# Performance work log

Measured on AMD Instinct MI355X. Metric: run time of the kernel, lower is better.

## Reference

```python
import jax, jax.numpy as jnp
import numpy as np

B, N, F_IN, F_OUT = 8, 256, 64, 64
EPS = 1e-12


def _mlp(x, w1, b1, w2, b2):
    # Dense -> ReLU -> Dense -> ReLU
    h = jax.nn.relu(x @ w1 + b1)
    return jax.nn.relu(h @ w2 + b2)


def setup_inputs() -> dict:
    key = jax.random.key(0)
    ks = jax.random.split(key, 11)
    A = jax.random.uniform(ks[0], (B, N, N), dtype=jnp.float32)
    W = jax.random.normal(ks[1], (B, N, N, F_OUT), dtype=jnp.float32)
    x = jax.random.normal(ks[2], (B, N, F_IN), dtype=jnp.float32)
    sc_in = 1.0 / np.sqrt(F_IN)
    sc_out = 1.0 / np.sqrt(F_OUT)
    return {
        "A": A, "W": W, "x": x,
        # n_func params
        "n_w1": jax.random.normal(ks[3], (F_IN, F_OUT), dtype=jnp.float32) * sc_in,
        "n_b1": jnp.zeros((F_OUT,), dtype=jnp.float32),
        "n_w2": jax.random.normal(ks[4], (F_OUT, F_OUT), dtype=jnp.float32) * sc_out,
        "n_b2": jnp.zeros((F_OUT,), dtype=jnp.float32),
        # n_self_func params
        "s_w1": jax.random.normal(ks[5], (F_IN, F_OUT), dtype=jnp.float32) * sc_in,
        "s_b1": jnp.zeros((F_OUT,), dtype=jnp.float32),
        "s_w2": jax.random.normal(ks[6], (F_OUT, F_OUT), dtype=jnp.float32) * sc_out,
        "s_b2": jnp.zeros((F_OUT,), dtype=jnp.float32),
    }


def reference(A, W, x, n_w1, n_b1, n_w2, n_b2, s_w1, s_b1, s_w2, s_b2):
    # L1 normalize adjacency over neighbor axis (axis=2)
    denom = jnp.maximum(jnp.sum(jnp.abs(A), axis=2, keepdims=True), EPS)
    An = A / denom  # [B,N,N]
    x1 = _mlp(x, n_w1, n_b1, n_w2, n_b2)  # [B,N,F_OUT]
    # (A[...,None]*W) transposed matmul with x1 == per-channel weighted aggregation:
    # x2[b,i,e] = sum_j An[b,i,j] * W[b,i,j,e] * x1[b,j,e]
    x2 = jnp.einsum('bij,bije,bje->bie', An, W, x1)
    x2 = x2 + _mlp(x, s_w1, s_b1, s_w2, s_b2)
    return (W, x2)
```

## Files before the change

### kernel.cpp

```cpp
#include <hip/hip_runtime.h>

#define NN    256
#define FF    64
#define BROWS 2048
#define W_ELEMS 33554432

typedef float v4f __attribute__((ext_vector_type(4)));

__global__ __launch_bounds__(64) void mlp_kernel(
    const float* __restrict__ x,
    const float* __restrict__ nw1, const float* __restrict__ nb1,
    const float* __restrict__ nw2, const float* __restrict__ nb2,
    const float* __restrict__ sw1, const float* __restrict__ sb1,
    const float* __restrict__ sw2, const float* __restrict__ sb2,
    float* __restrict__ x1, float* __restrict__ sout)
{
    const int row = blockIdx.x;
    const int e   = threadIdx.x;

    __shared__ float xr[FF];
    __shared__ float h[FF];

    xr[e] = x[row * FF + e];
    __syncthreads();

    float acc = nb1[e];
#pragma unroll
    for (int k = 0; k < FF; ++k) acc = fmaf(xr[k], nw1[k * FF + e], acc);
    h[e] = fmaxf(acc, 0.0f);
    __syncthreads();

    acc = nb2[e];
#pragma unroll
    for (int k = 0; k < FF; ++k) acc = fmaf(h[k], nw2[k * FF + e], acc);
    x1[row * FF + e] = fmaxf(acc, 0.0f);
    __syncthreads();

    acc = sb1[e];
#pragma unroll
    for (int k = 0; k < FF; ++k) acc = fmaf(xr[k], sw1[k * FF + e], acc);
    h[e] = fmaxf(acc, 0.0f);
    __syncthreads();

    acc = sb2[e];
#pragma unroll
    for (int k = 0; k < FF; ++k) acc = fmaf(h[k], sw2[k * FF + e], acc);
    sout[row * FF + e] = fmaxf(acc, 0.0f);
}

__global__ __launch_bounds__(256, 4) void agg_kernel(
    const float* __restrict__ A, const float* __restrict__ W,
    const float* __restrict__ x1, const float* __restrict__ sout,
    float* __restrict__ outW, float* __restrict__ outx2)
{
    const int row = blockIdx.x;
    const int b   = row >> 8;
    const int tid = threadIdx.x;

    __shared__ float an[NN];
    __shared__ float partial[4];
    __shared__ float red[256][4];

    const float a = A[row * NN + tid];
    float s = fabsf(a);
#pragma unroll
    for (int off = 32; off > 0; off >>= 1) s += __shfl_down(s, off, 64);
    if ((tid & 63) == 0) partial[tid >> 6] = s;
    __syncthreads();
    const float denom = fmaxf(partial[0] + partial[1] + partial[2] + partial[3], 1e-12f);
    an[tid] = a / denom;
    __syncthreads();

    const v4f* __restrict__ Wrow = (const v4f*)(W + (size_t)row * (NN * FF));
    v4f* __restrict__ Orow       = (v4f*)(outW + (size_t)row * (NN * FF));
    const v4f* __restrict__ x1b  = (const v4f*)(x1 + b * (NN * FF));

    const int jg = tid >> 4;

    float acc0 = 0.0f, acc1 = 0.0f, acc2 = 0.0f, acc3 = 0.0f;

#define LOADG(wp, xp, cbase)                                                  \
    _Pragma("unroll")                                                         \
    for (int q = 0; q < 4; ++q) {                                             \
        wp[q] = __builtin_nontemporal_load(Wrow + (cbase) + q * 256 + tid);   \
        xp[q] = x1b[(cbase) + q * 256 + tid];                                 \
    }

#define USEG(wp, xp, cbase, jjb)                                              \
    _Pragma("unroll")                                                         \
    for (int q = 0; q < 4; ++q) {                                             \
        __builtin_nontemporal_store(wp[q], Orow + (cbase) + q * 256 + tid);   \
    }                                                                         \
    _Pragma("unroll")                                                         \
    for (int q = 0; q < 4; ++q) {                                             \
        const float av = an[((jjb) + q) * 16 + jg];                           \
        acc0 = fmaf(av * wp[q].x, xp[q].x, acc0);                             \
        acc1 = fmaf(av * wp[q].y, xp[q].y, acc1);                             \
        acc2 = fmaf(av * wp[q].z, xp[q].z, acc2);                             \
        acc3 = fmaf(av * wp[q].w, xp[q].w, acc3);                             \
    }

    v4f wA[4], xA[4];
    v4f wB[4], xB[4];

    LOADG(wA, xA, 0)
    LOADG(wB, xB, 1024)
    USEG (wA, xA, 0, 0)
    LOADG(wA, xA, 2048)
    USEG (wB, xB, 1024, 4)
    LOADG(wB, xB, 3072)
    USEG (wA, xA, 2048, 8)
    USEG (wB, xB, 3072, 12)

#undef LOADG
#undef USEG

    red[tid][0] = acc0; red[tid][1] = acc1;
    red[tid][2] = acc2; red[tid][3] = acc3;
    __syncthreads();

    if (tid < 64) {
        const int c = tid >> 2;
        const int r = tid & 3;
        float sum = 0.0f;
#pragma unroll
        for (int g = 0; g < 16; ++g) sum += red[g * 16 + c][r];
        sum += sout[row * FF + tid];
        outx2[row * FF + tid] = sum;
    }
}

extern "C" void kernel_launch(void* const* d_in, const int* in_sizes, int n_in,
                              void* d_out, int out_size, void* d_ws, size_t ws_size,
                              hipStream_t stream) {
    const float* A   = (const float*)d_in[0];
    const float* W   = (const float*)d_in[1];
    const float* x   = (const float*)d_in[2];
    const float* nw1 = (const float*)d_in[3];
    const float* nb1 = (const float*)d_in[4];
    const float* nw2 = (const float*)d_in[5];
    const float* nb2 = (const float*)d_in[6];
    const float* sw1 = (const float*)d_in[7];
    const float* sb1 = (const float*)d_in[8];
    const float* sw2 = (const float*)d_in[9];
    const float* sb2 = (const float*)d_in[10];

    float* x1 = (float*)d_ws;
    float* so = x1 + BROWS * FF;

    float* outW  = (float*)d_out;
    float* outx2 = outW + W_ELEMS;

    mlp_kernel<<<BROWS, 64, 0, stream>>>(x, nw1, nb1, nw2, nb2,
                                         sw1, sb1, sw2, sb2, x1, so);
    agg_kernel<<<BROWS, 256, 0, stream>>>(A, W, x1, so, outW, outx2);
}
```

Measured before the change: 253.1 us.

## Split W passthrough copy into separate kernel and slim aggregation kernel

The W-to-output copy moves out of the aggregation kernel into a dedicated copy kernel launched afterward. The aggregation kernel now only reads W with normal cached loads, uses smaller double-buffered register groups, and asks for higher occupancy. The likely intent is that W stays in the large last-level cache after aggregation so the copy kernel re-reads it cheaply, while each kernel keeps a simpler access stream. The cost is an extra launch and a second read of the 128MB W tensor, which may not fit in cache and could add DRAM traffic.

```diff
diff --git a/kernel.cpp b/kernel.cpp
--- a/kernel.cpp
+++ b/kernel.cpp
@@ -48,10 +48,10 @@
     sout[row * FF + e] = fmaxf(acc, 0.0f);
 }
 
-__global__ __launch_bounds__(256, 4) void agg_kernel(
+__global__ __launch_bounds__(256, 8) void agg_kernel(
     const float* __restrict__ A, const float* __restrict__ W,
     const float* __restrict__ x1, const float* __restrict__ sout,
-    float* __restrict__ outW, float* __restrict__ outx2)
+    float* __restrict__ outx2)
 {
     const int row = blockIdx.x;
     const int b   = row >> 8;
@@ -72,7 +72,6 @@
     __syncthreads();
 
     const v4f* __restrict__ Wrow = (const v4f*)(W + (size_t)row * (NN * FF));
-    v4f* __restrict__ Orow       = (v4f*)(outW + (size_t)row * (NN * FF));
     const v4f* __restrict__ x1b  = (const v4f*)(x1 + b * (NN * FF));
 
     const int jg = tid >> 4;
@@ -81,18 +80,14 @@
 
 #define LOADG(wp, xp, cbase)                                                  \
     _Pragma("unroll")                                                         \
-    for (int q = 0; q < 4; ++q) {                                             \
-        wp[q] = __builtin_nontemporal_load(Wrow + (cbase) + q * 256 + tid);   \
+    for (int q = 0; q < 2; ++q) {                                             \
+        wp[q] = Wrow[(cbase) + q * 256 + tid];                                \
         xp[q] = x1b[(cbase) + q * 256 + tid];                                 \
     }
 
-#define USEG(wp, xp, cbase, jjb)                                              \
+#define USEG(wp, xp, jjb)                                                     \
     _Pragma("unroll")                                                         \
-    for (int q = 0; q < 4; ++q) {                                             \
-        __builtin_nontemporal_store(wp[q], Orow + (cbase) + q * 256 + tid);   \
-    }                                                                         \
-    _Pragma("unroll")                                                         \
-    for (int q = 0; q < 4; ++q) {                                             \
+    for (int q = 0; q < 2; ++q) {                                             \
         const float av = an[((jjb) + q) * 16 + jg];                           \
         acc0 = fmaf(av * wp[q].x, xp[q].x, acc0);                             \
         acc1 = fmaf(av * wp[q].y, xp[q].y, acc1);                             \
@@ -100,17 +95,18 @@
         acc3 = fmaf(av * wp[q].w, xp[q].w, acc3);                             \
     }
 
-    v4f wA[4], xA[4];
-    v4f wB[4], xB[4];
+    v4f wA[2], xA[2], wB[2], xB[2];
 
     LOADG(wA, xA, 0)
-    LOADG(wB, xB, 1024)
-    USEG (wA, xA, 0, 0)
-    LOADG(wA, xA, 2048)
-    USEG (wB, xB, 1024, 4)
-    LOADG(wB, xB, 3072)
-    USEG (wA, xA, 2048, 8)
-    USEG (wB, xB, 3072, 12)
+    LOADG(wB, xB, 512)
+    USEG (wA, xA, 0)   LOADG(wA, xA, 1024)
+    USEG (wB, xB, 2)   LOADG(wB, xB, 1536)
+    USEG (wA, xA, 4)   LOADG(wA, xA, 2048)
+    USEG (wB, xB, 6)   LOADG(wB, xB, 2560)
+    USEG (wA, xA, 8)   LOADG(wA, xA, 3072)
+    USEG (wB, xB, 10)  LOADG(wB, xB, 3584)
+    USEG (wA, xA, 12)
+    USEG (wB, xB, 14)
 
 #undef LOADG
 #undef USEG
@@ -127,6 +123,25 @@
         for (int g = 0; g < 16; ++g) sum += red[g * 16 + c][r];
         sum += sout[row * FF + tid];
         outx2[row * FF + tid] = sum;
+    }
+}
+
+__global__ __launch_bounds__(256) void copyw_kernel(
+    const float* __restrict__ src, float* __restrict__ dst)
+{
+    const v4f* __restrict__ s = (const v4f*)src;
+    v4f*       __restrict__ d = (v4f*)dst;
+    const int base = blockIdx.x * 4096 + threadIdx.x;
+
+    v4f t[8];
+#pragma unroll
+    for (int h = 0; h < 2; ++h) {
+#pragma unroll
+        for (int k = 0; k < 8; ++k)
+            t[k] = s[base + (h * 8 + k) * 256];
+#pragma unroll
+        for (int k = 0; k < 8; ++k)
+            __builtin_nontemporal_store(t[k], d + base + (h * 8 + k) * 256);
     }
 }
 
@@ -153,5 +168,6 @@
 
     mlp_kernel<<<BROWS, 64, 0, stream>>>(x, nw1, nb1, nw2, nb2,
                                          sw1, sb1, sw2, sb2, x1, so);
-    agg_kernel<<<BROWS, 256, 0, stream>>>(A, W, x1, so, outW, outx2);
+    agg_kernel<<<BROWS, 256, 0, stream>>>(A, W, x1, so, outx2);
+    copyw_kernel<<<BROWS, 256, 0, stream>>>(W, outW);
 }
```

Result: slower. 275.3 us (+8.8%).
